# Optimization experiments

Hardware: AMD Instinct MI355X
Metric: run time of the kernel (lower is better)

## Reference

```python
import jax, jax.numpy as jnp
import numpy as np

D_PAIR = 128
C = 128
EPS = 1e-5

def _ln(x, g, b):
    mu = jnp.mean(x, axis=-1, keepdims=True)
    var = jnp.var(x, axis=-1, keepdims=True)
    return (x - mu) * jax.lax.rsqrt(var + EPS) * g + b

def setup_inputs() -> dict:
    key = jax.random.key(0)
    ks = jax.random.split(key, 8)
    B, N, d, c = 1, 512, D_PAIR, C
    glorot = lambda k, fo, fi: jax.random.uniform(k, (fo, fi), jnp.float32,
                                                  -1.0, 1.0) * np.sqrt(6.0 / (fi + fo))
    return {
        "Z_raw": jax.random.normal(ks[0], (B, N, N, d), jnp.float32),
        "Z_mask_row": jnp.ones((B, N, N), jnp.float32),
        "ln1_g": jnp.ones((d,), jnp.float32),
        "ln1_b": jnp.zeros((d,), jnp.float32),
        "W_lr": glorot(ks[1], 2 * c, d),
        "b_lr": jnp.zeros((2 * c,), jnp.float32),
        "W_gate": jnp.zeros((2 * c, d), jnp.float32),   # initializer='zeros'
        "b_gate": jnp.ones((2 * c,), jnp.float32),      # bias_init=1.0
        "W_og": jnp.zeros((d, d), jnp.float32),
        "b_og": jnp.ones((d,), jnp.float32),
        "ln2_g": jnp.ones((c,), jnp.float32),
        "ln2_b": jnp.zeros((c,), jnp.float32),
        "W_out": jnp.zeros((d, d), jnp.float32),        # no bias
        "out_bias": jnp.zeros((d,), jnp.float32),
    }

def reference(Z_raw, Z_mask_row, ln1_g, ln1_b, W_lr, b_lr, W_gate, b_gate,
              W_og, b_og, ln2_g, ln2_b, W_out, out_bias):
    c = C
    Z = _ln(Z_raw, ln1_g, ln1_b)                         # [B,I,J,d]
    lr = jnp.einsum('bijd,ed->bije', Z, W_lr) + b_lr      # [B,I,J,2c]
    lr = Z_mask_row[..., None] * lr
    lr = lr * jax.nn.sigmoid(jnp.einsum('bijd,ed->bije', Z, W_gate) + b_gate)
    left, right = lr[..., :c], lr[..., c:]
    # triangle outgoing: p[b,i,j,c] = sum_k left[b,i,k,c] * right[b,j,k,c]
    p = jnp.einsum('bikc,bjkc->bijc', left, right)
    ab = jnp.einsum('bijc,ec->bije', _ln(p, ln2_g, ln2_b), W_out)
    g = jax.nn.sigmoid(jnp.einsum('bijd,ed->bije', Z, W_og) + b_og)
    # eval-mode bias_ele_dropout_residual (dropout mask = ones)
    return Z_raw + g * (ab + out_bias)
```

## Files before the change

### kernel.cpp

```cpp
#include <hip/hip_runtime.h>

#define NPOS 262144

typedef __attribute__((ext_vector_type(8))) short short8;
typedef __attribute__((ext_vector_type(4))) float f32x4;
typedef __attribute__((ext_vector_type(4))) unsigned short us4;
typedef __attribute__((ext_vector_type(4))) unsigned int u32x4;

__device__ __forceinline__ unsigned short f2bf(float f){
  unsigned u = __float_as_uint(f);
  u += 0x7fffu + ((u >> 16) & 1u);
  return (unsigned short)(u >> 16);
}
__device__ __forceinline__ float bf2f(unsigned int h){ return __uint_as_float(h << 16); }
__device__ __forceinline__ float sigm(float x){ return 1.f/(1.f + __expf(-x)); }

#define MFMA16(a,b,c) __builtin_amdgcn_mfma_f32_16x16x32_bf16((a),(b),(c),0,0,0)

__global__ __launch_bounds__(256) void k_prep(
    const float* __restrict__ Wlr, const float* __restrict__ b_lr,
    const float* __restrict__ Wg,  const float* __restrict__ b_g,
    const float* __restrict__ Wog, const float* __restrict__ b_og,
    const float* __restrict__ Wout,const float* __restrict__ obias,
    const float* __restrict__ g1, const float* __restrict__ b1,
    const float* __restrict__ g2, const float* __restrict__ b2,
    unsigned short* __restrict__ Wc, float* __restrict__ svec, float* __restrict__ cvec)
{
  int r = blockIdx.x*4 + (threadIdx.x >> 6);
  int l = threadIdx.x & 63;
  const float *W, *gv, *bv; float extra;
  if (r < 256)      { W = Wlr + r*128;         extra = b_lr[r];      gv=g1; bv=b1; }
  else if (r < 512) { W = Wg  + (r-256)*128;   extra = b_g[r-256];   gv=g1; bv=b1; }
  else if (r < 640) { W = Wog + (r-512)*128;   extra = b_og[r-512];  gv=g1; bv=b1; }
  else              { W = Wout+ (r-640)*128;   extra = obias[r-640]; gv=g2; bv=b2; }
  float w0 = W[2*l], w1 = W[2*l+1];
  float p0 = w0 * gv[2*l], p1 = w1 * gv[2*l+1];
  float s  = p0 + p1;
  float cc = w0 * bv[2*l] + w1 * bv[2*l+1];
  Wc[r*128 + 2*l]   = f2bf(p0);
  Wc[r*128 + 2*l+1] = f2bf(p1);
  for (int off=32; off; off>>=1){ s += __shfl_down(s, off); cc += __shfl_down(cc, off); }
  if (l == 0){ svec[r] = s; cvec[r] = cc + extra; }
}

__global__ __launch_bounds__(256, 3) void k_proj(
    const float* __restrict__ Zraw, const float* __restrict__ Zmask,
    const unsigned short* __restrict__ Wc,
    const float* __restrict__ svec, const float* __restrict__ cvec,
    unsigned short* __restrict__ leftT, unsigned short* __restrict__ rightT)
{
  __shared__ unsigned short zt[128*136];
  __shared__ unsigned short tlc[64*132];
  __shared__ float mu_s[128], rs_s[128], mask_s[128];
  const int t = threadIdx.x, l = t & 63, w = t >> 6;
  const int wr = w >> 1, wc = w & 1;
  const long pos0 = (long)blockIdx.x * 128;

  if (t < 128) mask_s[t] = Zmask[pos0 + t];
  { const f32x4* zg = (const f32x4*)(Zraw + pos0*128);
    f32x4 zv[16];
    #pragma unroll
    for (int v=0; v<16; v++) zv[v] = zg[v*256 + t];
    #pragma unroll
    for (int v=0; v<16; v++){
      int f = v*256 + t, row = f>>5, c4 = f&31;
      f32x4 z = zv[v];
      us4 h; h[0]=f2bf(z[0]); h[1]=f2bf(z[1]); h[2]=f2bf(z[2]); h[3]=f2bf(z[3]);
      *(us4*)&zt[row*136 + c4*4] = h;
      float s  = (z[0]+z[1]) + (z[2]+z[3]);
      float ss = (z[0]*z[0]+z[1]*z[1]) + (z[2]*z[2]+z[3]*z[3]);
      #pragma unroll
      for (int off=16; off; off>>=1){ s += __shfl_xor(s, off); ss += __shfl_xor(ss, off); }
      if ((l&31) == 0){
        float mu = s * 0.0078125f;
        float var = ss * 0.0078125f - mu*mu;
        mu_s[row] = mu; rs_s[row] = rsqrtf(var + 1e-5f);
      }
    }
  }
  __syncthreads();

  for (int half=0; half<2; half++){
    const unsigned short* Blr = Wc + (half*128)*128;
    const unsigned short* Bgt = Wc + (256 + half*128)*128;
    for (int np=0; np<2; np++){
      f32x4 accL[4][2], accG[4][2];
      #pragma unroll
      for (int mt=0; mt<4; mt++)
        #pragma unroll
        for (int nt=0; nt<2; nt++){
          accL[mt][nt] = (f32x4)(0.f); accG[mt][nt] = (f32x4)(0.f);
        }
      #pragma unroll
      for (int ks=0; ks<4; ks++){
        const int krow = ks*32 + ((l>>4)<<3);
        short8 bl[2], bg[2];
        #pragma unroll
        for (int nt=0; nt<2; nt++){
          int n = wc*64 + np*32 + nt*16 + (l&15);
          bl[nt] = *(const short8*)(Blr + n*128 + krow);
          bg[nt] = *(const short8*)(Bgt + n*128 + krow);
        }
        #pragma unroll
        for (int mt=0; mt<4; mt++){
          int row = wr*64 + mt*16 + (l&15);
          short8 a = *(const short8*)&zt[row*136 + krow];
          #pragma unroll
          for (int nt=0; nt<2; nt++){
            accL[mt][nt] = MFMA16(a, bl[nt], accL[mt][nt]);
            accG[mt][nt] = MFMA16(a, bg[nt], accG[mt][nt]);
          }
        }
      }
      #pragma unroll
      for (int nt=0; nt<2; nt++){
        int col = wc*64 + np*32 + nt*16 + (l&15);
        float sL = svec[half*128 + col],       cL = cvec[half*128 + col];
        float sG = svec[256 + half*128 + col], cG = cvec[256 + half*128 + col];
        int cc = wc*32 + nt*16 + (l&15);
        #pragma unroll
        for (int mt=0; mt<4; mt++){
          int rowb = wr*64 + mt*16 + ((l>>4)<<2);
          us4 h;
          #pragma unroll
          for (int r=0; r<4; r++){
            int row = rowb + r;
            float rs = rs_s[row], rm = rs*mu_s[row];
            float lrv = rs*accL[mt][nt][r] - rm*sL + cL;
            float gv  = sigm(rs*accG[mt][nt][r] - rm*sG + cG);
            h[r] = f2bf(mask_s[row] * lrv * gv);
          }
          *(us4*)&tlc[cc*132 + rowb] = h;
        }
      }
      __syncthreads();
      unsigned short* dst = half ? rightT : leftT;
      #pragma unroll
      for (int v=0; v<16; v++){
        int f2 = v*256 + t, cc = f2>>6, rp = (f2&63)<<1;
        int col = ((cc>>5)<<6) + np*32 + (cc&31);
        unsigned u = *(const unsigned*)&tlc[cc*132 + rp];
        *(unsigned*)&dst[(long)col*NPOS + pos0 + rp] = u;
      }
      __syncthreads();
    }
  }
}

__global__ __launch_bounds__(256) void k_tri(
    const unsigned short* __restrict__ leftT, const unsigned short* __restrict__ rightT,
    unsigned short* __restrict__ pP)
{
  __shared__ unsigned short At[128*72];
  __shared__ unsigned short Bt[128*72];
  __shared__ unsigned short pj[128*132];
  const int t = threadIdx.x, l = t & 63, w = t >> 6;
  const int wr = w >> 1, wc = w & 1;
  const int c = blockIdx.x >> 4, tile = blockIdx.x & 15;
  const int ti = (tile >> 2) << 7, tj = (tile & 3) << 7;
  const unsigned short* L = leftT  + (long)c*NPOS + (long)ti*512;
  const unsigned short* R = rightT + (long)c*NPOS + (long)tj*512;
  f32x4 acc[4][4];
  for (int mt=0; mt<4; mt++) for (int nt=0; nt<4; nt++) acc[mt][nt] = (f32x4)(0.f);
  for (int kt=0; kt<8; kt++){
    const int k0 = kt*64;
    __syncthreads();
    for (int v=0; v<4; v++){
      int f = v*256 + t, row = f>>3, kc = f&7;
      *(u32x4*)&At[row*72 + kc*8] = *(const u32x4*)(L + row*512 + k0 + kc*8);
      *(u32x4*)&Bt[row*72 + kc*8] = *(const u32x4*)(R + row*512 + k0 + kc*8);
    }
    __syncthreads();
    for (int ks2=0; ks2<2; ks2++){
      const int krow = ks2*32 + ((l>>4)<<3);
      short8 br[4];
      for (int nt=0; nt<4; nt++)
        br[nt] = *(const short8*)&Bt[(wc*64 + nt*16 + (l&15))*72 + krow];
      for (int mt=0; mt<4; mt++){
        short8 a = *(const short8*)&At[(wr*64 + mt*16 + (l&15))*72 + krow];
        for (int nt=0; nt<4; nt++)
          acc[mt][nt] = MFMA16(a, br[nt], acc[mt][nt]);
      }
    }
  }
  __syncthreads();
  for (int mt=0; mt<4; mt++){
    int rowb = wr*64 + mt*16 + ((l>>4)<<2);
    for (int nt=0; nt<4; nt++){
      int col = wc*64 + nt*16 + (l&15);
      for (int r=0; r<4; r++)
        pj[(rowb+r)*132 + col] = f2bf(acc[mt][nt][r]);
    }
  }
  __syncthreads();
  unsigned short* dst = pP + (long)c*NPOS + (long)ti*512 + tj;
  for (int v=0; v<32; v++){
    int f2 = v*256 + t, row = f2>>6, cp = (f2&63)<<1;
    unsigned u = *(const unsigned*)&pj[row*132 + cp];
    *(unsigned*)&dst[(long)row*512 + cp] = u;
  }
}

__global__ __launch_bounds__(256) void k_out(
    const float* __restrict__ Zraw, const unsigned short* __restrict__ pP,
    const unsigned short* __restrict__ Wc,
    const float* __restrict__ svec, const float* __restrict__ cvec,
    float* __restrict__ out)
{
  __shared__ unsigned short zt[128*144];
  __shared__ unsigned pt[128*65];
  __shared__ float sb[256*4];
  __shared__ float mu1s[128], rs1s[128], mu2s[128], rs2s[128];
  const int t = threadIdx.x, l = t & 63, w = t >> 6;
  const int wr = w >> 1, wc = w & 1;
  const long pos0 = (long)blockIdx.x * 128;
  const int ib = blockIdx.x >> 2, j0 = (blockIdx.x & 3) << 7;

  { const f32x4* zg = (const f32x4*)(Zraw + pos0*128);
    for (int v=0; v<16; v++){
      int f = v*256 + t, row = f>>5, c4 = f&31;
      f32x4 z = zg[f];
      us4 h; h[0]=f2bf(z[0]); h[1]=f2bf(z[1]); h[2]=f2bf(z[2]); h[3]=f2bf(z[3]);
      *(us4*)&zt[row*144 + c4*4] = h;
    }
  }
  for (int v=0; v<32; v++){
    int f = v*256 + t, cch = f>>6, j2 = f&63;
    pt[cch*65 + j2] = *(const unsigned*)&pP[(long)cch*NPOS + (long)ib*512 + j0 + 2*j2];
  }
  __syncthreads();

  {
    int sr = t & 127, hi = t >> 7;
    float s=0.f, ss=0.f;
    for (int it=hi*32; it<hi*32+32; it++){
      int c2 = (sr + it) & 63;
      unsigned u = *(const unsigned*)&zt[sr*144 + c2*2];
      float a = bf2f(u & 0xffffu), b = bf2f(u >> 16);
      s += a + b; ss += a*a + b*b;
    }
    sb[t*4+0] = s; sb[t*4+1] = ss;
    int jp = t & 63, ch = t >> 6;
    float s0=0.f, ss0=0.f, s1=0.f, ss1=0.f;
    for (int cc=ch*32; cc<ch*32+32; cc++){
      unsigned u = pt[cc*65 + jp];
      float a = bf2f(u & 0xffffu), b = bf2f(u >> 16);
      s0 += a; ss0 += a*a; s1 += b; ss1 += b*b;
    }
    __syncthreads();
    if (t < 128){
      float S = sb[t*4+0] + sb[(t+128)*4+0];
      float SS = sb[t*4+1] + sb[(t+128)*4+1];
      float mu = S*0.0078125f, var = SS*0.0078125f - mu*mu;
      mu1s[t] = mu; rs1s[t] = rsqrtf(var + 1e-5f);
    }
    __syncthreads();
    sb[t*4+0] = s0; sb[t*4+1] = ss0; sb[t*4+2] = s1; sb[t*4+3] = ss1;
    __syncthreads();
    if (t >= 128){
      int j = t - 128, jpp = j >> 1, o = j & 1;
      float S=0.f, SS=0.f;
      for (int ww=0; ww<4; ww++){
        S  += sb[(ww*64 + jpp)*4 + 2*o];
        SS += sb[(ww*64 + jpp)*4 + 2*o + 1];
      }
      float mu = S*0.0078125f, var = SS*0.0078125f - mu*mu;
      mu2s[j] = mu; rs2s[j] = rsqrtf(var + 1e-5f);
    }
  }
  __syncthreads();

  const unsigned short* W2  = Wc + 640*128;
  const unsigned short* WgB = Wc + 512*128;
  const unsigned short* pt16 = (const unsigned short*)pt;
  f32x4 acc1[4][4], acc2[4][4];
  for (int mt=0; mt<4; mt++) for (int nt=0; nt<4; nt++){
    acc1[mt][nt]=(f32x4)(0.f); acc2[mt][nt]=(f32x4)(0.f);
  }
  for (int ks=0; ks<4; ks++){
    const int krow = ks*32 + ((l>>4)<<3);
    short8 bo[4], bg[4];
    for (int nt=0; nt<4; nt++){
      int n = wc*64 + nt*16 + (l&15);
      bo[nt] = *(const short8*)(W2  + n*128 + krow);
      bg[nt] = *(const short8*)(WgB + n*128 + krow);
    }
    for (int mt=0; mt<4; mt++){
      int row = wr*64 + mt*16 + (l&15);
      short8 ap;
      #pragma unroll
      for (int m=0; m<8; m++)
        ap[m] = (short)pt16[(krow+m)*130 + row];
      short8 az = *(const short8*)&zt[row*144 + krow];
      for (int nt=0; nt<4; nt++){
        acc1[mt][nt] = MFMA16(ap, bo[nt], acc1[mt][nt]);
        acc2[mt][nt] = MFMA16(az, bg[nt], acc2[mt][nt]);
      }
    }
  }
  for (int mt=0; mt<4; mt++){
    int rowb = wr*64 + mt*16 + ((l>>4)<<2);
    for (int nt=0; nt<4; nt++){
      int col = wc*64 + nt*16 + (l&15);
      float sO = svec[640 + col], cO = cvec[640 + col];
      float sg = svec[512 + col], cg = cvec[512 + col];
      for (int r=0; r<4; r++){
        int row = rowb + r;
        float ab = rs2s[row]*acc1[mt][nt][r] - rs2s[row]*mu2s[row]*sO + cO;
        float gv = sigm(rs1s[row]*acc2[mt][nt][r] - rs1s[row]*mu1s[row]*sg + cg);
        long gidx = (pos0 + row)*128 + col;
        out[gidx] = Zraw[gidx] + gv*ab;
      }
    }
  }
}

extern "C" void kernel_launch(void* const* d_in, const int* in_sizes, int n_in,
                              void* d_out, int out_size, void* d_ws, size_t ws_size,
                              hipStream_t stream)
{
  (void)in_sizes; (void)n_in; (void)out_size; (void)ws_size;
  const float* Zraw  = (const float*)d_in[0];
  const float* Zmask = (const float*)d_in[1];
  const float* g1    = (const float*)d_in[2];
  const float* b1    = (const float*)d_in[3];
  const float* Wlr   = (const float*)d_in[4];
  const float* blr   = (const float*)d_in[5];
  const float* Wg    = (const float*)d_in[6];
  const float* bg    = (const float*)d_in[7];
  const float* Wog   = (const float*)d_in[8];
  const float* bog   = (const float*)d_in[9];
  const float* g2    = (const float*)d_in[10];
  const float* b2    = (const float*)d_in[11];
  const float* Wout  = (const float*)d_in[12];
  const float* obias = (const float*)d_in[13];

  char* ws = (char*)d_ws;
  unsigned short* leftT  = (unsigned short*)(ws);
  unsigned short* rightT = (unsigned short*)(ws + 67108864L);
  unsigned short* pP     = (unsigned short*)(ws + 134217728L);
  unsigned short* Wc     = (unsigned short*)(ws + 201326592L);
  float* svec            = (float*)(ws + 201326592L + 196608L);
  float* cvec            = (float*)(ws + 201326592L + 196608L + 4096L);
  float* out = (float*)d_out;

  k_prep<<<192, 256, 0, stream>>>(Wlr, blr, Wg, bg, Wog, bog, Wout, obias,
                                  g1, b1, g2, b2, Wc, svec, cvec);
  k_proj<<<2048, 256, 0, stream>>>(Zraw, Zmask, Wc, svec, cvec, leftT, rightT);
  k_tri<<<2048, 256, 0, stream>>>(leftT, rightT, pP);
  k_out<<<2048, 256, 0, stream>>>(Zraw, pP, Wc, svec, cvec, out);
}
```

Baseline: 551.7 us.

## Shrink tiles and LDS use across kernels to raise occupancy, remap tri blocks per XCD

k_proj now processes 64 positions per block instead of 128, which cuts its LDS footprint and doubles the grid, and it targets four waves per SIMD. k_tri aliases the output staging buffer onto the A/B tile buffers to reduce LDS, and it remaps block IDs so each XCD handles a contiguous set of channels for better L2 locality. k_out drops the bf16 Z tile in LDS. It fuses the pair-LN statistics into the pP load, recomputes bf16 Z operands directly from global memory, and splits the N dimension into two passes to lower register pressure. The cost is extra global reads of Z in k_out and more blocks doing redundant weight loads.

```diff
diff --git a/kernel.cpp b/kernel.cpp
--- a/kernel.cpp
+++ b/kernel.cpp
@@ -43,30 +43,30 @@
   if (l == 0){ svec[r] = s; cvec[r] = cc + extra; }
 }
 
-__global__ __launch_bounds__(256, 3) void k_proj(
+__global__ __launch_bounds__(256, 4) void k_proj(
     const float* __restrict__ Zraw, const float* __restrict__ Zmask,
     const unsigned short* __restrict__ Wc,
     const float* __restrict__ svec, const float* __restrict__ cvec,
     unsigned short* __restrict__ leftT, unsigned short* __restrict__ rightT)
 {
-  __shared__ unsigned short zt[128*136];
-  __shared__ unsigned short tlc[64*132];
-  __shared__ float mu_s[128], rs_s[128], mask_s[128];
+  __shared__ unsigned short zt[64*144];
+  __shared__ unsigned short tlc[64*68];
+  __shared__ float mu_s[64], rs_s[64], mask_s[64];
   const int t = threadIdx.x, l = t & 63, w = t >> 6;
   const int wr = w >> 1, wc = w & 1;
-  const long pos0 = (long)blockIdx.x * 128;
-
-  if (t < 128) mask_s[t] = Zmask[pos0 + t];
+  const long pos0 = (long)blockIdx.x * 64;
+
+  if (t < 64) mask_s[t] = Zmask[pos0 + t];
   { const f32x4* zg = (const f32x4*)(Zraw + pos0*128);
-    f32x4 zv[16];
-    #pragma unroll
-    for (int v=0; v<16; v++) zv[v] = zg[v*256 + t];
-    #pragma unroll
-    for (int v=0; v<16; v++){
+    f32x4 zv[8];
+    #pragma unroll
+    for (int v=0; v<8; v++) zv[v] = zg[v*256 + t];
+    #pragma unroll
+    for (int v=0; v<8; v++){
       int f = v*256 + t, row = f>>5, c4 = f&31;
       f32x4 z = zv[v];
       us4 h; h[0]=f2bf(z[0]); h[1]=f2bf(z[1]); h[2]=f2bf(z[2]); h[3]=f2bf(z[3]);
-      *(us4*)&zt[row*136 + c4*4] = h;
+      *(us4*)&zt[row*144 + c4*4] = h;
       float s  = (z[0]+z[1]) + (z[2]+z[3]);
       float ss = (z[0]*z[0]+z[1]*z[1]) + (z[2]*z[2]+z[3]*z[3]);
       #pragma unroll
@@ -81,12 +81,12 @@
   __syncthreads();
 
   for (int half=0; half<2; half++){
-    const unsigned short* Blr = Wc + (half*128)*128;
-    const unsigned short* Bgt = Wc + (256 + half*128)*128;
     for (int np=0; np<2; np++){
-      f32x4 accL[4][2], accG[4][2];
-      #pragma unroll
-      for (int mt=0; mt<4; mt++)
+      const unsigned short* Blr = Wc + (half*128 + np*64 + wc*32)*128;
+      const unsigned short* Bgt = Blr + 256*128;
+      f32x4 accL[2][2], accG[2][2];
+      #pragma unroll
+      for (int mt=0; mt<2; mt++)
         #pragma unroll
         for (int nt=0; nt<2; nt++){
           accL[mt][nt] = (f32x4)(0.f); accG[mt][nt] = (f32x4)(0.f);
@@ -97,14 +97,14 @@
         short8 bl[2], bg[2];
         #pragma unroll
         for (int nt=0; nt<2; nt++){
-          int n = wc*64 + np*32 + nt*16 + (l&15);
+          int n = nt*16 + (l&15);
           bl[nt] = *(const short8*)(Blr + n*128 + krow);
           bg[nt] = *(const short8*)(Bgt + n*128 + krow);
         }
         #pragma unroll
-        for (int mt=0; mt<4; mt++){
-          int row = wr*64 + mt*16 + (l&15);
-          short8 a = *(const short8*)&zt[row*136 + krow];
+        for (int mt=0; mt<2; mt++){
+          int row = wr*32 + mt*16 + (l&15);
+          short8 a = *(const short8*)&zt[row*144 + krow];
           #pragma unroll
           for (int nt=0; nt<2; nt++){
             accL[mt][nt] = MFMA16(a, bl[nt], accL[mt][nt]);
@@ -112,51 +112,59 @@
           }
         }
       }
-      #pragma unroll
-      for (int nt=0; nt<2; nt++){
-        int col = wc*64 + np*32 + nt*16 + (l&15);
-        float sL = svec[half*128 + col],       cL = cvec[half*128 + col];
-        float sG = svec[256 + half*128 + col], cG = cvec[256 + half*128 + col];
-        int cc = wc*32 + nt*16 + (l&15);
-        #pragma unroll
-        for (int mt=0; mt<4; mt++){
-          int rowb = wr*64 + mt*16 + ((l>>4)<<2);
-          us4 h;
+      {
+        int cbase = wc*32 + (l&15);
+        int nn0 = np*64 + cbase, nn1 = nn0 + 16;
+        float sL0 = svec[half*128 + nn0], cL0 = cvec[half*128 + nn0];
+        float sL1 = svec[half*128 + nn1], cL1 = cvec[half*128 + nn1];
+        float sG0 = svec[256 + half*128 + nn0], cG0 = cvec[256 + half*128 + nn0];
+        float sG1 = svec[256 + half*128 + nn1], cG1 = cvec[256 + half*128 + nn1];
+        #pragma unroll
+        for (int mt=0; mt<2; mt++){
+          int rowb = wr*32 + mt*16 + ((l>>4)<<2);
+          us4 h0, h1;
           #pragma unroll
           for (int r=0; r<4; r++){
             int row = rowb + r;
-            float rs = rs_s[row], rm = rs*mu_s[row];
-            float lrv = rs*accL[mt][nt][r] - rm*sL + cL;
-            float gv  = sigm(rs*accG[mt][nt][r] - rm*sG + cG);
-            h[r] = f2bf(mask_s[row] * lrv * gv);
+            float rs = rs_s[row], rm = rs*mu_s[row], mk = mask_s[row];
+            float l0 = rs*accL[mt][0][r] - rm*sL0 + cL0;
+            float g0 = sigm(rs*accG[mt][0][r] - rm*sG0 + cG0);
+            h0[r] = f2bf(mk * l0 * g0);
+            float l1 = rs*accL[mt][1][r] - rm*sL1 + cL1;
+            float g1 = sigm(rs*accG[mt][1][r] - rm*sG1 + cG1);
+            h1[r] = f2bf(mk * l1 * g1);
           }
-          *(us4*)&tlc[cc*132 + rowb] = h;
+          *(us4*)&tlc[cbase*68 + rowb] = h0;
+          *(us4*)&tlc[(cbase+16)*68 + rowb] = h1;
         }
       }
       __syncthreads();
       unsigned short* dst = half ? rightT : leftT;
       #pragma unroll
-      for (int v=0; v<16; v++){
-        int f2 = v*256 + t, cc = f2>>6, rp = (f2&63)<<1;
-        int col = ((cc>>5)<<6) + np*32 + (cc&31);
-        unsigned u = *(const unsigned*)&tlc[cc*132 + rp];
-        *(unsigned*)&dst[(long)col*NPOS + pos0 + rp] = u;
+      for (int v=0; v<8; v++){
+        int f2 = v*256 + t, cc = f2>>5, rp = (f2&31)<<1;
+        unsigned u = *(const unsigned*)&tlc[cc*68 + rp];
+        *(unsigned*)&dst[(long)(np*64 + cc)*NPOS + pos0 + rp] = u;
       }
       __syncthreads();
     }
   }
 }
 
-__global__ __launch_bounds__(256) void k_tri(
+__global__ __launch_bounds__(256, 4) void k_tri(
     const unsigned short* __restrict__ leftT, const unsigned short* __restrict__ rightT,
     unsigned short* __restrict__ pP)
 {
-  __shared__ unsigned short At[128*72];
-  __shared__ unsigned short Bt[128*72];
-  __shared__ unsigned short pj[128*132];
+  __shared__ unsigned short smem[2*128*72];
+  unsigned short* At = smem;
+  unsigned short* Bt = smem + 128*72;
+  unsigned short* pj = smem;
   const int t = threadIdx.x, l = t & 63, w = t >> 6;
   const int wr = w >> 1, wc = w & 1;
-  const int c = blockIdx.x >> 4, tile = blockIdx.x & 15;
+  const int bid = blockIdx.x;
+  const int xcd = bid & 7, q = bid >> 3;
+  const int c = (xcd << 4) | (q & 15);
+  const int tile = q >> 4;
   const int ti = (tile >> 2) << 7, tj = (tile & 3) << 7;
   const unsigned short* L = leftT  + (long)c*NPOS + (long)ti*512;
   const unsigned short* R = rightT + (long)c*NPOS + (long)tj*512;
@@ -201,13 +209,12 @@
   }
 }
 
-__global__ __launch_bounds__(256) void k_out(
+__global__ __launch_bounds__(256, 3) void k_out(
     const float* __restrict__ Zraw, const unsigned short* __restrict__ pP,
     const unsigned short* __restrict__ Wc,
     const float* __restrict__ svec, const float* __restrict__ cvec,
     float* __restrict__ out)
 {
-  __shared__ unsigned short zt[128*144];
   __shared__ unsigned pt[128*65];
   __shared__ float sb[256*4];
   __shared__ float mu1s[128], rs1s[128], mu2s[128], rs2s[128];
@@ -216,100 +223,107 @@
   const long pos0 = (long)blockIdx.x * 128;
   const int ib = blockIdx.x >> 2, j0 = (blockIdx.x & 3) << 7;
 
-  { const f32x4* zg = (const f32x4*)(Zraw + pos0*128);
-    for (int v=0; v<16; v++){
-      int f = v*256 + t, row = f>>5, c4 = f&31;
-      f32x4 z = zg[f];
-      us4 h; h[0]=f2bf(z[0]); h[1]=f2bf(z[1]); h[2]=f2bf(z[2]); h[3]=f2bf(z[3]);
-      *(us4*)&zt[row*144 + c4*4] = h;
-    }
-  }
+  float s0=0.f, ss0=0.f, s1=0.f, ss1=0.f;
+  #pragma unroll
   for (int v=0; v<32; v++){
     int f = v*256 + t, cch = f>>6, j2 = f&63;
-    pt[cch*65 + j2] = *(const unsigned*)&pP[(long)cch*NPOS + (long)ib*512 + j0 + 2*j2];
-  }
-  __syncthreads();
-
-  {
-    int sr = t & 127, hi = t >> 7;
-    float s=0.f, ss=0.f;
-    for (int it=hi*32; it<hi*32+32; it++){
-      int c2 = (sr + it) & 63;
-      unsigned u = *(const unsigned*)&zt[sr*144 + c2*2];
-      float a = bf2f(u & 0xffffu), b = bf2f(u >> 16);
-      s += a + b; ss += a*a + b*b;
-    }
-    sb[t*4+0] = s; sb[t*4+1] = ss;
-    int jp = t & 63, ch = t >> 6;
-    float s0=0.f, ss0=0.f, s1=0.f, ss1=0.f;
-    for (int cc=ch*32; cc<ch*32+32; cc++){
-      unsigned u = pt[cc*65 + jp];
-      float a = bf2f(u & 0xffffu), b = bf2f(u >> 16);
-      s0 += a; ss0 += a*a; s1 += b; ss1 += b*b;
-    }
-    __syncthreads();
-    if (t < 128){
-      float S = sb[t*4+0] + sb[(t+128)*4+0];
-      float SS = sb[t*4+1] + sb[(t+128)*4+1];
-      float mu = S*0.0078125f, var = SS*0.0078125f - mu*mu;
-      mu1s[t] = mu; rs1s[t] = rsqrtf(var + 1e-5f);
-    }
-    __syncthreads();
-    sb[t*4+0] = s0; sb[t*4+1] = ss0; sb[t*4+2] = s1; sb[t*4+3] = ss1;
-    __syncthreads();
-    if (t >= 128){
-      int j = t - 128, jpp = j >> 1, o = j & 1;
-      float S=0.f, SS=0.f;
-      for (int ww=0; ww<4; ww++){
-        S  += sb[(ww*64 + jpp)*4 + 2*o];
-        SS += sb[(ww*64 + jpp)*4 + 2*o + 1];
-      }
-      float mu = S*0.0078125f, var = SS*0.0078125f - mu*mu;
-      mu2s[j] = mu; rs2s[j] = rsqrtf(var + 1e-5f);
-    }
-  }
-  __syncthreads();
-
-  const unsigned short* W2  = Wc + 640*128;
-  const unsigned short* WgB = Wc + 512*128;
+    unsigned u = *(const unsigned*)&pP[(long)cch*NPOS + (long)ib*512 + j0 + 2*j2];
+    pt[cch*65 + j2] = u;
+    float a = bf2f(u & 0xffffu), b = bf2f(u >> 16);
+    s0 += a; ss0 += a*a; s1 += b; ss1 += b*b;
+  }
+  { const f32x4* zg = (const f32x4*)(Zraw + pos0*128);
+    #pragma unroll
+    for (int v=0; v<16; v++){
+      int f = v*256 + t, row = f>>5;
+      f32x4 z = zg[f];
+      float s  = (z[0]+z[1]) + (z[2]+z[3]);
+      float ss = (z[0]*z[0]+z[1]*z[1]) + (z[2]*z[2]+z[3]*z[3]);
+      #pragma unroll
+      for (int off=16; off; off>>=1){ s += __shfl_xor(s, off); ss += __shfl_xor(ss, off); }
+      if ((l&31) == 0){
+        float mu = s * 0.0078125f;
+        float var = ss * 0.0078125f - mu*mu;
+        mu1s[row] = mu; rs1s[row] = rsqrtf(var + 1e-5f);
+      }
+    }
+  }
+  sb[t*4+0] = s0; sb[t*4+1] = ss0; sb[t*4+2] = s1; sb[t*4+3] = ss1;
+  __syncthreads();
+  if (t < 128){
+    int j = t, jpp = j >> 1, o = j & 1;
+    float S=0.f, SS=0.f;
+    #pragma unroll
+    for (int ww=0; ww<4; ww++){
+      S  += sb[(ww*64 + jpp)*4 + 2*o];
+      SS += sb[(ww*64 + jpp)*4 + 2*o + 1];
+    }
+    float mu = S*0.0078125f, var = SS*0.0078125f - mu*mu;
+    mu2s[j] = mu; rs2s[j] = rsqrtf(var + 1e-5f);
+  }
+  __syncthreads();
+
   const unsigned short* pt16 = (const unsigned short*)pt;
-  f32x4 acc1[4][4], acc2[4][4];
-  for (int mt=0; mt<4; mt++) for (int nt=0; nt<4; nt++){
-    acc1[mt][nt]=(f32x4)(0.f); acc2[mt][nt]=(f32x4)(0.f);
-  }
-  for (int ks=0; ks<4; ks++){
-    const int krow = ks*32 + ((l>>4)<<3);
-    short8 bo[4], bg[4];
-    for (int nt=0; nt<4; nt++){
-      int n = wc*64 + nt*16 + (l&15);
-      bo[nt] = *(const short8*)(W2  + n*128 + krow);
-      bg[nt] = *(const short8*)(WgB + n*128 + krow);
-    }
+  const float* zbase = Zraw + pos0*128;
+  for (int np=0; np<2; np++){
+    f32x4 acc1[4][2], acc2[4][2];
+    #pragma unroll
+    for (int mt=0; mt<4; mt++)
+      #pragma unroll
+      for (int nt=0; nt<2; nt++){
+        acc1[mt][nt]=(f32x4)(0.f); acc2[mt][nt]=(f32x4)(0.f);
+      }
+    #pragma unroll
+    for (int ks=0; ks<4; ks++){
+      const int krow = ks*32 + ((l>>4)<<3);
+      short8 bo[2], bg[2];
+      #pragma unroll
+      for (int nt=0; nt<2; nt++){
+        int n = np*64 + wc*32 + nt*16 + (l&15);
+        bo[nt] = *(const short8*)(Wc + (640+n)*128 + krow);
+        bg[nt] = *(const short8*)(Wc + (512+n)*128 + krow);
+      }
+      #pragma unroll
+      for (int mt=0; mt<4; mt++){
+        int row = wr*64 + mt*16 + (l&15);
+        short8 ap;
+        #pragma unroll
+        for (int m=0; m<8; m++)
+          ap[m] = (short)pt16[(krow+m)*130 + row];
+        const float* zp = zbase + row*128 + krow;
+        f32x4 za = *(const f32x4*)zp, zb2 = *(const f32x4*)(zp+4);
+        short8 az;
+        az[0]=(short)f2bf(za[0]); az[1]=(short)f2bf(za[1]);
+        az[2]=(short)f2bf(za[2]); az[3]=(short)f2bf(za[3]);
+        az[4]=(short)f2bf(zb2[0]); az[5]=(short)f2bf(zb2[1]);
+        az[6]=(short)f2bf(zb2[2]); az[7]=(short)f2bf(zb2[3]);
+        #pragma unroll
+        for (int nt=0; nt<2; nt++){
+          acc1[mt][nt] = MFMA16(ap, bo[nt], acc1[mt][nt]);
+          acc2[mt][nt] = MFMA16(az, bg[nt], acc2[mt][nt]);
+        }
+      }
+    }
+    int cbase = np*64 + wc*32 + (l&15);
+    float sO0 = svec[640 + cbase],      cO0 = cvec[640 + cbase];
+    float sO1 = svec[640 + cbase + 16], cO1 = cvec[640 + cbase + 16];
+    float sg0 = svec[512 + cbase],      cg0 = cvec[512 + cbase];
+    float sg1 = svec[512 + cbase + 16], cg1 = cvec[512 + cbase + 16];
+    #pragma unroll
     for (int mt=0; mt<4; mt++){
-      int row = wr*64 + mt*16 + (l&15);
-      short8 ap;
-      #pragma unroll
-      for (int m=0; m<8; m++)
-        ap[m] = (short)pt16[(krow+m)*130 + row];
-      short8 az = *(const short8*)&zt[row*144 + krow];
-      for (int nt=0; nt<4; nt++){
-        acc1[mt][nt] = MFMA16(ap, bo[nt], acc1[mt][nt]);
-        acc2[mt][nt] = MFMA16(az, bg[nt], acc2[mt][nt]);
-      }
-    }
-  }
-  for (int mt=0; mt<4; mt++){
-    int rowb = wr*64 + mt*16 + ((l>>4)<<2);
-    for (int nt=0; nt<4; nt++){
-      int col = wc*64 + nt*16 + (l&15);
-      float sO = svec[640 + col], cO = cvec[640 + col];
-      float sg = svec[512 + col], cg = cvec[512 + col];
+      int rowb = wr*64 + mt*16 + ((l>>4)<<2);
+      #pragma unroll
       for (int r=0; r<4; r++){
         int row = rowb + r;
-        float ab = rs2s[row]*acc1[mt][nt][r] - rs2s[row]*mu2s[row]*sO + cO;
-        float gv = sigm(rs1s[row]*acc2[mt][nt][r] - rs1s[row]*mu1s[row]*sg + cg);
-        long gidx = (pos0 + row)*128 + col;
-        out[gidx] = Zraw[gidx] + gv*ab;
+        float rs2 = rs2s[row], rm2 = rs2*mu2s[row];
+        float rs1 = rs1s[row], rm1 = rs1*mu1s[row];
+        long gidx = (pos0 + row)*128;
+        float ab0 = rs2*acc1[mt][0][r] - rm2*sO0 + cO0;
+        float gv0 = sigm(rs1*acc2[mt][0][r] - rm1*sg0 + cg0);
+        out[gidx + cbase] = Zraw[gidx + cbase] + gv0*ab0;
+        float ab1 = rs2*acc1[mt][1][r] - rm2*sO1 + cO1;
+        float gv1 = sigm(rs1*acc2[mt][1][r] - rm1*sg1 + cg1);
+        out[gidx + cbase + 16] = Zraw[gidx + cbase + 16] + gv1*ab1;
       }
     }
   }
@@ -346,7 +360,7 @@
 
   k_prep<<<192, 256, 0, stream>>>(Wlr, blr, Wg, bg, Wog, bog, Wout, obias,
                                   g1, b1, g2, b2, Wc, svec, cvec);
-  k_proj<<<2048, 256, 0, stream>>>(Zraw, Zmask, Wc, svec, cvec, leftT, rightT);
+  k_proj<<<4096, 256, 0, stream>>>(Zraw, Zmask, Wc, svec, cvec, leftT, rightT);
   k_tri<<<2048, 256, 0, stream>>>(leftT, rightT, pP);
   k_out<<<2048, 256, 0, stream>>>(Zraw, pP, Wc, svec, cvec, out);
 }
```

Measured after the change: 788.3 us. 1.43x slower.

## Transpose p tile into swizzled LDS layout and fuse LN stats into loads

Applied to the files above, without the earlier changes.

In k_out, the p tile is stored transposed in shared memory with an XOR swizzle, so the MFMA A-operand becomes one 16-byte vector read instead of eight scalar strided reads. LN1 and LN2 statistics are now computed during the global loads with shuffles, which removes the separate reduction pass and several barriers. k_tri reuses one shared buffer for the A/B tiles and the output staging and requests 4 blocks per CU through launch bounds to raise occupancy. The added unrolling and the occupancy hint may increase register pressure or cause spills.

```diff
diff --git a/kernel.cpp b/kernel.cpp
--- a/kernel.cpp
+++ b/kernel.cpp
@@ -81,8 +81,6 @@
   __syncthreads();
 
   for (int half=0; half<2; half++){
-    const unsigned short* Blr = Wc + (half*128)*128;
-    const unsigned short* Bgt = Wc + (256 + half*128)*128;
     for (int np=0; np<2; np++){
       f32x4 accL[4][2], accG[4][2];
       #pragma unroll
@@ -91,6 +89,8 @@
         for (int nt=0; nt<2; nt++){
           accL[mt][nt] = (f32x4)(0.f); accG[mt][nt] = (f32x4)(0.f);
         }
+      const unsigned short* Blr = Wc + (half*128)*128;
+      const unsigned short* Bgt = Wc + (256 + half*128)*128;
       #pragma unroll
       for (int ks=0; ks<4; ks++){
         const int krow = ks*32 + ((l>>4)<<3);
@@ -147,13 +147,14 @@
   }
 }
 
-__global__ __launch_bounds__(256) void k_tri(
+__global__ __launch_bounds__(256, 4) void k_tri(
     const unsigned short* __restrict__ leftT, const unsigned short* __restrict__ rightT,
     unsigned short* __restrict__ pP)
 {
-  __shared__ unsigned short At[128*72];
-  __shared__ unsigned short Bt[128*72];
-  __shared__ unsigned short pj[128*132];
+  __shared__ unsigned short smem[2*128*72];
+  unsigned short* At = smem;
+  unsigned short* Bt = smem + 128*72;
+  unsigned short* pj = smem;
   const int t = threadIdx.x, l = t & 63, w = t >> 6;
   const int wr = w >> 1, wc = w & 1;
   const int c = blockIdx.x >> 4, tile = blockIdx.x & 15;
@@ -208,7 +209,7 @@
     float* __restrict__ out)
 {
   __shared__ unsigned short zt[128*144];
-  __shared__ unsigned pt[128*65];
+  __shared__ unsigned short ptT[128*136];
   __shared__ float sb[256*4];
   __shared__ float mu1s[128], rs1s[128], mu2s[128], rs2s[128];
   const int t = threadIdx.x, l = t & 63, w = t >> 6;
@@ -217,81 +218,73 @@
   const int ib = blockIdx.x >> 2, j0 = (blockIdx.x & 3) << 7;
 
   { const f32x4* zg = (const f32x4*)(Zraw + pos0*128);
+    #pragma unroll
     for (int v=0; v<16; v++){
       int f = v*256 + t, row = f>>5, c4 = f&31;
       f32x4 z = zg[f];
       us4 h; h[0]=f2bf(z[0]); h[1]=f2bf(z[1]); h[2]=f2bf(z[2]); h[3]=f2bf(z[3]);
       *(us4*)&zt[row*144 + c4*4] = h;
-    }
-  }
+      float s  = (z[0]+z[1]) + (z[2]+z[3]);
+      float ss = (z[0]*z[0]+z[1]*z[1]) + (z[2]*z[2]+z[3]*z[3]);
+      #pragma unroll
+      for (int off=16; off; off>>=1){ s += __shfl_xor(s, off); ss += __shfl_xor(ss, off); }
+      if ((l&31) == 0){
+        float mu = s * 0.0078125f;
+        float var = ss * 0.0078125f - mu*mu;
+        mu1s[row] = mu; rs1s[row] = rsqrtf(var + 1e-5f);
+      }
+    }
+  }
+  float s0=0.f, ss0=0.f, s1=0.f, ss1=0.f;
+  #pragma unroll
   for (int v=0; v<32; v++){
     int f = v*256 + t, cch = f>>6, j2 = f&63;
-    pt[cch*65 + j2] = *(const unsigned*)&pP[(long)cch*NPOS + (long)ib*512 + j0 + 2*j2];
-  }
-  __syncthreads();
-
-  {
-    int sr = t & 127, hi = t >> 7;
-    float s=0.f, ss=0.f;
-    for (int it=hi*32; it<hi*32+32; it++){
-      int c2 = (sr + it) & 63;
-      unsigned u = *(const unsigned*)&zt[sr*144 + c2*2];
-      float a = bf2f(u & 0xffffu), b = bf2f(u >> 16);
-      s += a + b; ss += a*a + b*b;
-    }
-    sb[t*4+0] = s; sb[t*4+1] = ss;
-    int jp = t & 63, ch = t >> 6;
-    float s0=0.f, ss0=0.f, s1=0.f, ss1=0.f;
-    for (int cc=ch*32; cc<ch*32+32; cc++){
-      unsigned u = pt[cc*65 + jp];
-      float a = bf2f(u & 0xffffu), b = bf2f(u >> 16);
-      s0 += a; ss0 += a*a; s1 += b; ss1 += b*b;
-    }
-    __syncthreads();
-    if (t < 128){
-      float S = sb[t*4+0] + sb[(t+128)*4+0];
-      float SS = sb[t*4+1] + sb[(t+128)*4+1];
-      float mu = S*0.0078125f, var = SS*0.0078125f - mu*mu;
-      mu1s[t] = mu; rs1s[t] = rsqrtf(var + 1e-5f);
-    }
-    __syncthreads();
-    sb[t*4+0] = s0; sb[t*4+1] = ss0; sb[t*4+2] = s1; sb[t*4+3] = ss1;
-    __syncthreads();
-    if (t >= 128){
-      int j = t - 128, jpp = j >> 1, o = j & 1;
-      float S=0.f, SS=0.f;
-      for (int ww=0; ww<4; ww++){
-        S  += sb[(ww*64 + jpp)*4 + 2*o];
-        SS += sb[(ww*64 + jpp)*4 + 2*o + 1];
-      }
-      float mu = S*0.0078125f, var = SS*0.0078125f - mu*mu;
-      mu2s[j] = mu; rs2s[j] = rsqrtf(var + 1e-5f);
-    }
+    unsigned u = *(const unsigned*)&pP[(long)cch*NPOS + (long)ib*512 + j0 + 2*j2];
+    int q  = (j2 >> 2) & 7;
+    int cs = cch ^ (q << 3);
+    ptT[(2*j2)*136 + cs]   = (unsigned short)(u & 0xffffu);
+    ptT[(2*j2+1)*136 + cs] = (unsigned short)(u >> 16);
+    float a = bf2f(u & 0xffffu), b = bf2f(u >> 16);
+    s0 += a; ss0 += a*a; s1 += b; ss1 += b*b;
+  }
+  sb[t*4+0] = s0; sb[t*4+1] = ss0; sb[t*4+2] = s1; sb[t*4+3] = ss1;
+  __syncthreads();
+  if (t < 128){
+    int j = t, jpp = j >> 1, o = j & 1;
+    float S=0.f, SS=0.f;
+    #pragma unroll
+    for (int ww=0; ww<4; ww++){
+      S  += sb[(ww*64 + jpp)*4 + 2*o];
+      SS += sb[(ww*64 + jpp)*4 + 2*o + 1];
+    }
+    float mu = S*0.0078125f, var = SS*0.0078125f - mu*mu;
+    mu2s[j] = mu; rs2s[j] = rsqrtf(var + 1e-5f);
   }
   __syncthreads();
 
   const unsigned short* W2  = Wc + 640*128;
   const unsigned short* WgB = Wc + 512*128;
-  const unsigned short* pt16 = (const unsigned short*)pt;
   f32x4 acc1[4][4], acc2[4][4];
   for (int mt=0; mt<4; mt++) for (int nt=0; nt<4; nt++){
     acc1[mt][nt]=(f32x4)(0.f); acc2[mt][nt]=(f32x4)(0.f);
   }
+  #pragma unroll
   for (int ks=0; ks<4; ks++){
     const int krow = ks*32 + ((l>>4)<<3);
     short8 bo[4], bg[4];
+    #pragma unroll
     for (int nt=0; nt<4; nt++){
       int n = wc*64 + nt*16 + (l&15);
       bo[nt] = *(const short8*)(W2  + n*128 + krow);
       bg[nt] = *(const short8*)(WgB + n*128 + krow);
     }
+    #pragma unroll
     for (int mt=0; mt<4; mt++){
       int row = wr*64 + mt*16 + (l&15);
-      short8 ap;
-      #pragma unroll
-      for (int m=0; m<8; m++)
-        ap[m] = (short)pt16[(krow+m)*130 + row];
+      int qs = (row >> 3) & 7;
+      short8 ap = *(const short8*)&ptT[row*136 + (krow ^ (qs << 3))];
       short8 az = *(const short8*)&zt[row*144 + krow];
+      #pragma unroll
       for (int nt=0; nt<4; nt++){
         acc1[mt][nt] = MFMA16(ap, bo[nt], acc1[mt][nt]);
         acc2[mt][nt] = MFMA16(az, bg[nt], acc2[mt][nt]);
```

After: 725.3 us. 1.31x slower.
